# Kernel optimization log

Measured on AMD Instinct MI355X. Metric: run time of the kernel, lower is better.

## Reference

```python
import jax, jax.numpy as jnp
import numpy as np

T, B, D, H, NQ = 512, 256, 256, 256, 4  # note H == B is required by the original torch broadcasting


def setup_inputs() -> dict:
    key = jax.random.key(0)
    ks = jax.random.split(key, 9)
    inp = {"inputs": jax.random.normal(ks[0], (T, B, D), jnp.float32)}
    names = ["forget", "input", "update", "output"]
    for j, n in enumerate(names):
        inp[f"W_{n}"] = jax.random.normal(ks[1 + j], (NQ, D + H), jnp.float32) * 0.05
        inp[f"b_{n}"] = jnp.zeros((NQ,), jnp.float32)
        inp[f"phi_{n}"] = jax.random.uniform(ks[5 + j], (NQ,), jnp.float32, 0.0, 2.0 * np.pi)
    return inp


def _qgate(z, phi):
    # 4-qubit circuit on |0000>: RX(z_j) then trainable RX(phi_j) on each wire
    # (two RX on the same wire compose: angle theta_j = z_j + phi_j), then the
    # CNOT ring (0->1,1->2,2->3,3->0), then <Z_0>.
    # Heisenberg picture: conjugating Z_0 back through the CNOT ring gives
    # Z_0 -> Z_1 Z_2 Z_3, and on the product state <Z_j> = cos(theta_j), so
    # <Z_0> = cos(theta_1) * cos(theta_2) * cos(theta_3)  (wire 0 drops out).
    c = jnp.cos(z + phi)  # [B, 4]
    return c[:, 1] * c[:, 2] * c[:, 3]  # [B]


def reference(inputs, W_forget, b_forget, phi_forget, W_input, b_input, phi_input,
              W_update, b_update, phi_update, W_output, b_output, phi_output):
    bsz = inputs.shape[1]
    hx = jnp.zeros((bsz, H), inputs.dtype)
    cx = jnp.zeros((bsz, H), inputs.dtype)

    def step(carry, x):
        hx, cx = carry
        comb = jnp.concatenate([x, hx], axis=1)  # [B, D+H]
        f = jax.nn.sigmoid(_qgate(comb @ W_forget.T + b_forget, phi_forget))   # [B]
        i = jax.nn.sigmoid(_qgate(comb @ W_input.T + b_input, phi_input))      # [B]
        g = jnp.tanh(_qgate(comb @ W_update.T + b_update, phi_update))         # [B]
        o = jax.nn.sigmoid(_qgate(comb @ W_output.T + b_output, phi_output))   # [B]
        # [B] * [B,H] broadcasts the gate over the hidden axis (valid since H == B,
        # exactly matching the original torch semantics)
        cx = f * cx + i * g
        hx = o * jnp.tanh(cx)
        return (hx, cx), hx

    (hx, cx), outs = jax.lax.scan(step, (hx, cx), inputs)
    return outs, hx, cx
```

## Files before the change

### kernel.cpp

```cpp
#include <hip/hip_runtime.h>


#define T_DIM 512
#define B_DIM 256
#define D_DIM 256
#define H_DIM 256
#define DH    512
#define NG    16
#define XPAD  68

typedef float f32x4 __attribute__((ext_vector_type(4)));

__device__ __forceinline__ float fast_sigmoid(float x) {
    return 1.0f / (1.0f + __expf(-x));
}
__device__ __forceinline__ float fast_tanh(float x) {
    float e = __expf(2.0f * x);
    return (e - 1.0f) / (e + 1.0f);
}
template <int CTRL, int RM, int BM, bool BC>
__device__ __forceinline__ float dadd(float x) {
    return x + __int_as_float(
        __builtin_amdgcn_update_dpp(0, __float_as_int(x), CTRL, RM, BM, BC));
}
__device__ __forceinline__ float wsum(float x) {
    x = dadd<0x111, 0xf, 0xf, true >(x);
    x = dadd<0x112, 0xf, 0xf, true >(x);
    x = dadd<0x114, 0xf, 0xf, true >(x);
    x = dadd<0x118, 0xf, 0xf, true >(x);
    x = dadd<0x142, 0xa, 0xf, false>(x);
    x = dadd<0x143, 0xc, 0xf, false>(x);
    return x;
}
__device__ __forceinline__ float dpp_xor1(float x) {
    return __int_as_float(
        __builtin_amdgcn_update_dpp(0, __float_as_int(x), 0xB1, 0xf, 0xf, true));
}
__device__ __forceinline__ void lds_barrier() {
    __asm__ volatile("s_waitcnt lgkmcnt(0)\n\ts_barrier" ::: "memory");
}

__global__ __launch_bounds__(256) void zx_kernel(
    const float* __restrict__ x,
    const float* __restrict__ Wf, const float* __restrict__ Wi,
    const float* __restrict__ Wu, const float* __restrict__ Wo,
    const float* __restrict__ bf, const float* __restrict__ bi,
    const float* __restrict__ bu, const float* __restrict__ bo,
    const float* __restrict__ phf, const float* __restrict__ phi,
    const float* __restrict__ phu, const float* __restrict__ pho,
    float* __restrict__ zx)
{
    __shared__ float Xc[256][XPAD];
    __shared__ float Wc[NG][XPAD];
    const int tid = threadIdx.x;
    const int rt  = tid >> 2;
    const int qt  = tid & 3;

    const float* bv = (qt == 0) ? bf : (qt == 1) ? bi : (qt == 2) ? bu : bo;
    const float* pv = (qt == 0) ? phf : (qt == 1) ? phi : (qt == 2) ? phu : pho;
    float acc[4][4];
    #pragma unroll
    for (int j = 0; j < 4; ++j) {
        const float bj = bv[j] + pv[j];
        acc[0][j] = bj; acc[1][j] = bj; acc[2][j] = bj; acc[3][j] = bj;
    }

    const long base = (long)blockIdx.x * 256 * D_DIM;

    for (int c = 0; c < 4; ++c) {
        const int k0 = c * 64;
        #pragma unroll
        for (int it = 0; it < 16; ++it) {
            const int e = tid + it * 256;
            const int row = e >> 4, col4 = (e & 15) * 4;
            *(float4*)&Xc[row][col4] =
                *(const float4*)(x + base + (long)row * D_DIM + k0 + col4);
        }
        {
            const int q16 = tid >> 4, col4 = (tid & 15) * 4;
            const int g = q16 >> 2, qj = q16 & 3;
            const float* W = (g == 0) ? Wf : (g == 1) ? Wi : (g == 2) ? Wu : Wo;
            *(float4*)&Wc[q16][col4] = *(const float4*)(W + qj * DH + k0 + col4);
        }
        __syncthreads();

        #pragma unroll 4
        for (int kk = 0; kk < 16; ++kk) {
            const int k4 = kk * 4;
            float4 xv0 = *(float4*)&Xc[rt][k4];
            float4 xv1 = *(float4*)&Xc[rt +  64][k4];
            float4 xv2 = *(float4*)&Xc[rt + 128][k4];
            float4 xv3 = *(float4*)&Xc[rt + 192][k4];
            float4 wv0 = *(float4*)&Wc[4 * qt + 0][k4];
            float4 wv1 = *(float4*)&Wc[4 * qt + 1][k4];
            float4 wv2 = *(float4*)&Wc[4 * qt + 2][k4];
            float4 wv3 = *(float4*)&Wc[4 * qt + 3][k4];
            #pragma unroll
            for (int i = 0; i < 4; ++i) {
                const float4 xv = (i == 0) ? xv0 : (i == 1) ? xv1 : (i == 2) ? xv2 : xv3;
                acc[i][0] = fmaf(xv.x, wv0.x, fmaf(xv.y, wv0.y, fmaf(xv.z, wv0.z, fmaf(xv.w, wv0.w, acc[i][0]))));
                acc[i][1] = fmaf(xv.x, wv1.x, fmaf(xv.y, wv1.y, fmaf(xv.z, wv1.z, fmaf(xv.w, wv1.w, acc[i][1]))));
                acc[i][2] = fmaf(xv.x, wv2.x, fmaf(xv.y, wv2.y, fmaf(xv.z, wv2.z, fmaf(xv.w, wv2.w, acc[i][2]))));
                acc[i][3] = fmaf(xv.x, wv3.x, fmaf(xv.y, wv3.y, fmaf(xv.z, wv3.z, fmaf(xv.w, wv3.w, acc[i][3]))));
            }
        }
        __syncthreads();
    }

    const long orow = (long)blockIdx.x * 256;
    #pragma unroll
    for (int i = 0; i < 4; ++i) {
        *(float4*)&zx[(orow + rt + 64 * i) * NG + qt * 4] =
            make_float4(acc[i][0], acc[i][1], acc[i][2], acc[i][3]);
    }
}

__global__ __launch_bounds__(512) void rec_kernel(
    const float* __restrict__ Wf, const float* __restrict__ Wi,
    const float* __restrict__ Wu, const float* __restrict__ Wo,
    const float* __restrict__ zx,
    float* __restrict__ hv_tab,
    float* __restrict__ c_fin)
{
    __shared__ float Hbuf[2][H_DIM];
    __shared__ __align__(16) float zh_s[2][8];
    const int tid  = threadIdx.x;
    const int lane = tid & 63;
    const int wv   = tid >> 6;
    const int h    = tid >> 1;
    const int half = tid & 1;
    const int l4   = lane * 4;

    float4 WA = make_float4(0,0,0,0), WB = WA;
    if (wv < 6) {
        const int cA = 2 * wv, cB = cA + 1;
        const int gA = cA / 3, jA = cA % 3 + 1;
        const int gB = cB / 3, jB = cB % 3 + 1;
        const float* WgA = (gA == 0) ? Wf : (gA == 1) ? Wi : (gA == 2) ? Wu : Wo;
        const float* WgB = (gB == 0) ? Wf : (gB == 1) ? Wi : (gB == 2) ? Wu : Wo;
        WA = *(const float4*)(WgA + jA * DH + 256 + l4);
        WB = *(const float4*)(WgB + jB * DH + 256 + l4);
    }

    float C = 0.0f, Hprev = 0.0f;
    if (tid < H_DIM) Hbuf[1][tid] = 0.0f;
    __syncthreads();

    float4 za0, za1, zb0, zb1;
    {
        const float4* p0 = (const float4*)(zx + (long)h * NG) + half * 2;
        const float4* p1 = (const float4*)(zx + ((long)B_DIM + h) * NG) + half * 2;
        za0 = p0[0]; za1 = p0[1];
        zb0 = p1[0]; zb1 = p1[1];
    }

    auto step = [&](int t, float4& z0, float4& z1) {
        if (half) hv_tab[(long)(t - 1) * H_DIM + h] = Hprev;

        if (wv < 6) {
            const float4 Hv4 = *(const float4*)&Hbuf[(t + 1) & 1][l4];
            float pA = fmaf(WA.x, Hv4.x, fmaf(WA.y, Hv4.y, fmaf(WA.z, Hv4.z, WA.w * Hv4.w)));
            float pB = fmaf(WB.x, Hv4.x, fmaf(WB.y, Hv4.y, fmaf(WB.z, Hv4.z, WB.w * Hv4.w)));
            pA = wsum(pA);
            pB = wsum(pB);
            if (lane == 63) {
                const int cA = 2 * wv;
                zh_s[cA / 6][cA % 6]             = pA;
                zh_s[(cA + 1) / 6][(cA + 1) % 6] = pB;
            }
        }
        lds_barrier();

        const float4 ZA = *(const float4*)&zh_s[half][0];
        const float2 ZB = *(const float2*)&zh_s[half][4];
        const float c1 = __cosf(z0.y + ZA.x), c2 = __cosf(z0.z + ZA.y), c3 = __cosf(z0.w + ZA.z);
        const float c4 = __cosf(z1.y + ZA.w), c5 = __cosf(z1.z + ZB.x), c6 = __cosf(z1.w + ZB.y);
        const float pA = c1 * c2 * c3, pB = c4 * c5 * c6;
        float gA, gB;
        if (half == 0) { gA = fast_sigmoid(pA); gB = fast_sigmoid(pB); }
        else           { gA = fast_tanh(pA);    gB = fast_sigmoid(pB); }
        const float oA = dpp_xor1(gA);
        const float oB = dpp_xor1(gB);
        const float f_ = half ? oA : gA;
        const float i_ = half ? oB : gB;
        const float g_ = half ? gA : oA;
        const float o_ = half ? gB : oB;

        {
            const int tp = (t + 2 < T_DIM) ? (t + 2) : t;
            const float4* pp = (const float4*)(zx + ((long)tp * B_DIM + h) * NG) + half * 2;
            z0 = pp[0]; z1 = pp[1];
        }

        C = fmaf(f_, C, i_ * g_);
        const float Hnew = o_ * fast_tanh(C);
        if (half == 0) Hbuf[t & 1][h] = Hnew;
        Hprev = Hnew;
        lds_barrier();
    };

    for (int t = 0; t < T_DIM; t += 2) {
        step(t,     za0, za1);
        step(t + 1, zb0, zb1);
    }

    if (half) {
        hv_tab[(long)(T_DIM - 1) * H_DIM + h] = Hprev;
        c_fin[h] = C;
    }
}

__global__ __launch_bounds__(256) void bc_kernel(
    const float* __restrict__ hv_tab, const float* __restrict__ c_fin,
    float* __restrict__ out)
{
    const int blk  = blockIdx.x;
    const int w    = threadIdx.x >> 6;
    const int lane = threadIdx.x & 63;

    const float* src;
    long base;
    int rbase;
    if (blk < 4 * T_DIM) {
        const int t = blk >> 2;
        rbase = (blk & 3) * 64;
        src = hv_tab + (long)t * H_DIM;
        base = (long)t * (B_DIM * H_DIM);
    } else {
        const int k = blk - 4 * T_DIM;
        rbase = (k & 3) * 64;
        src = (k < 4) ? (hv_tab + (long)(T_DIM - 1) * H_DIM) : c_fin;
        base = (long)T_DIM * (B_DIM * H_DIM) + (k < 4 ? 0 : (long)B_DIM * H_DIM);
    }
    const f32x4 v = ((const f32x4*)src)[lane];
    #pragma unroll
    for (int it = 0; it < 16; ++it) {
        const int row = rbase + w + 4 * it;
        __builtin_nontemporal_store(
            v, (f32x4*)(out + base + (long)row * H_DIM) + lane);
    }
}

extern "C" void kernel_launch(void* const* d_in, const int* in_sizes, int n_in,
                              void* d_out, int out_size, void* d_ws, size_t ws_size,
                              hipStream_t stream) {
    (void)in_sizes; (void)n_in; (void)out_size; (void)ws_size;
    const float* x   = (const float*)d_in[0];
    const float* Wf  = (const float*)d_in[1];
    const float* bf  = (const float*)d_in[2];
    const float* phf = (const float*)d_in[3];
    const float* Wi  = (const float*)d_in[4];
    const float* bi  = (const float*)d_in[5];
    const float* phi = (const float*)d_in[6];
    const float* Wu  = (const float*)d_in[7];
    const float* bu  = (const float*)d_in[8];
    const float* phu = (const float*)d_in[9];
    const float* Wo  = (const float*)d_in[10];
    const float* bo  = (const float*)d_in[11];
    const float* pho = (const float*)d_in[12];

    float* zx     = (float*)d_ws;
    float* hv_pad = zx + (size_t)T_DIM * B_DIM * NG;
    float* hv_tab = hv_pad + H_DIM;
    float* c_fin  = hv_tab + (size_t)T_DIM * H_DIM;

    zx_kernel<<<T_DIM, 256, 0, stream>>>(
        x, Wf, Wi, Wu, Wo, bf, bi, bu, bo, phf, phi, phu, pho, zx);

    rec_kernel<<<1, 512, 0, stream>>>(
        Wf, Wi, Wu, Wo, zx, hv_tab, c_fin);

    bc_kernel<<<4 * T_DIM + 8, 256, 0, stream>>>(hv_tab, c_fin, (float*)d_out);
}
```

Measured before the change: 599.6 us.

## Fuse broadcast into recurrence kernel with chunked flag-based producer-consumer overlap

Merges the broadcast kernel into the recurrent kernel. Block 0 runs the serial recurrence and publishes a release flag after each 32-step chunk of hidden states. The other blocks spin on those flags and write the broadcast output while the recurrence is still running. The aim is to hide the large broadcast write traffic behind the latency-bound serial scan. In exchange it relies on all blocks being co-resident (risk of deadlock otherwise), and the stores from consumer blocks may contend with the recurrence block.

```diff
diff --git a/kernel.cpp b/kernel.cpp
--- a/kernel.cpp
+++ b/kernel.cpp
@@ -8,6 +8,8 @@
 #define DH    512
 #define NG    16
 #define XPAD  68
+#define CHUNK 32
+#define NCHUNK (T_DIM / CHUNK)
 
 typedef float f32x4 __attribute__((ext_vector_type(4)));
 
@@ -39,6 +41,16 @@
 __device__ __forceinline__ void lds_barrier() {
     __asm__ volatile("s_waitcnt lgkmcnt(0)\n\ts_barrier" ::: "memory");
 }
+__device__ __forceinline__ void wait_flag(const int* f) {
+    if (threadIdx.x == 0) {
+        while (__hip_atomic_load(f, __ATOMIC_ACQUIRE,
+                                 __HIP_MEMORY_SCOPE_AGENT) == 0) {
+            __builtin_amdgcn_s_sleep(32);
+        }
+    }
+    __syncthreads();
+    __threadfence();
+}
 
 __global__ __launch_bounds__(256) void zx_kernel(
     const float* __restrict__ x,
@@ -48,13 +60,15 @@
     const float* __restrict__ bu, const float* __restrict__ bo,
     const float* __restrict__ phf, const float* __restrict__ phi,
     const float* __restrict__ phu, const float* __restrict__ pho,
-    float* __restrict__ zx)
+    float* __restrict__ zx, int* __restrict__ flags)
 {
     __shared__ float Xc[256][XPAD];
     __shared__ float Wc[NG][XPAD];
     const int tid = threadIdx.x;
     const int rt  = tid >> 2;
     const int qt  = tid & 3;
+
+    if (blockIdx.x == 0 && tid < NCHUNK) flags[tid] = 0;
 
     const float* bv = (qt == 0) ? bf : (qt == 1) ? bi : (qt == 2) ? bu : bo;
     const float* pv = (qt == 0) ? phf : (qt == 1) ? phi : (qt == 2) ? phu : pho;
@@ -115,16 +129,54 @@
     }
 }
 
-__global__ __launch_bounds__(512) void rec_kernel(
+__global__ __launch_bounds__(512, 8) void rec_bc_kernel(
     const float* __restrict__ Wf, const float* __restrict__ Wi,
     const float* __restrict__ Wu, const float* __restrict__ Wo,
     const float* __restrict__ zx,
     float* __restrict__ hv_tab,
-    float* __restrict__ c_fin)
+    float* __restrict__ c_fin,
+    int* __restrict__ flags,
+    float* __restrict__ out)
 {
+    const int tid  = threadIdx.x;
+
+    if (blockIdx.x != 0) {
+        const int lane = tid & 63;
+        const int w    = tid >> 6;
+
+        if (blockIdx.x <= 256) {
+            const int tb0 = 2 * ((int)blockIdx.x - 1);
+            wait_flag(&flags[tb0 >> 5]);
+            #pragma unroll
+            for (int tt = 0; tt < 2; ++tt) {
+                const int tb = tb0 + tt;
+                const f32x4 v = ((const f32x4*)(hv_tab + (long)tb * H_DIM))[lane];
+                const long base = (long)tb * (B_DIM * H_DIM);
+                #pragma unroll
+                for (int it = 0; it < 32; ++it) {
+                    const int row = w + 8 * it;
+                    __builtin_nontemporal_store(
+                        v, (f32x4*)(out + base + (long)row * H_DIM) + lane);
+                }
+            }
+        } else {
+            wait_flag(&flags[NCHUNK - 1]);
+            const f32x4 vh = ((const f32x4*)(hv_tab + (long)(T_DIM - 1) * H_DIM))[lane];
+            const f32x4 vc = ((const f32x4*)c_fin)[lane];
+            const long bh = (long)T_DIM * (B_DIM * H_DIM);
+            const long bc = bh + (long)B_DIM * H_DIM;
+            #pragma unroll
+            for (int it = 0; it < 32; ++it) {
+                const int row = w + 8 * it;
+                __builtin_nontemporal_store(vh, (f32x4*)(out + bh + (long)row * H_DIM) + lane);
+                __builtin_nontemporal_store(vc, (f32x4*)(out + bc + (long)row * H_DIM) + lane);
+            }
+        }
+        return;
+    }
+
     __shared__ float Hbuf[2][H_DIM];
     __shared__ __align__(16) float zh_s[2][8];
-    const int tid  = threadIdx.x;
     const int lane = tid & 63;
     const int wv   = tid >> 6;
     const int h    = tid >> 1;
@@ -202,42 +254,27 @@
     for (int t = 0; t < T_DIM; t += 2) {
         step(t,     za0, za1);
         step(t + 1, zb0, zb1);
+        if (t > 0 && (t & 31) == 0) {
+            __asm__ volatile("s_waitcnt vmcnt(0)" ::: "memory");
+            __syncthreads();
+            if (tid == 0) {
+                __threadfence();
+                __hip_atomic_store(&flags[(t >> 5) - 1], 1,
+                                   __ATOMIC_RELEASE, __HIP_MEMORY_SCOPE_AGENT);
+            }
+        }
     }
 
     if (half) {
         hv_tab[(long)(T_DIM - 1) * H_DIM + h] = Hprev;
         c_fin[h] = C;
     }
-}
-
-__global__ __launch_bounds__(256) void bc_kernel(
-    const float* __restrict__ hv_tab, const float* __restrict__ c_fin,
-    float* __restrict__ out)
-{
-    const int blk  = blockIdx.x;
-    const int w    = threadIdx.x >> 6;
-    const int lane = threadIdx.x & 63;
-
-    const float* src;
-    long base;
-    int rbase;
-    if (blk < 4 * T_DIM) {
-        const int t = blk >> 2;
-        rbase = (blk & 3) * 64;
-        src = hv_tab + (long)t * H_DIM;
-        base = (long)t * (B_DIM * H_DIM);
-    } else {
-        const int k = blk - 4 * T_DIM;
-        rbase = (k & 3) * 64;
-        src = (k < 4) ? (hv_tab + (long)(T_DIM - 1) * H_DIM) : c_fin;
-        base = (long)T_DIM * (B_DIM * H_DIM) + (k < 4 ? 0 : (long)B_DIM * H_DIM);
-    }
-    const f32x4 v = ((const f32x4*)src)[lane];
-    #pragma unroll
-    for (int it = 0; it < 16; ++it) {
-        const int row = rbase + w + 4 * it;
-        __builtin_nontemporal_store(
-            v, (f32x4*)(out + base + (long)row * H_DIM) + lane);
+    __asm__ volatile("s_waitcnt vmcnt(0)" ::: "memory");
+    __syncthreads();
+    if (tid == 0) {
+        __threadfence();
+        __hip_atomic_store(&flags[NCHUNK - 1], 1,
+                           __ATOMIC_RELEASE, __HIP_MEMORY_SCOPE_AGENT);
     }
 }
 
@@ -263,12 +300,11 @@
     float* hv_pad = zx + (size_t)T_DIM * B_DIM * NG;
     float* hv_tab = hv_pad + H_DIM;
     float* c_fin  = hv_tab + (size_t)T_DIM * H_DIM;
+    int*   flags  = (int*)(c_fin + H_DIM);
 
     zx_kernel<<<T_DIM, 256, 0, stream>>>(
-        x, Wf, Wi, Wu, Wo, bf, bi, bu, bo, phf, phi, phu, pho, zx);
-
-    rec_kernel<<<1, 512, 0, stream>>>(
-        Wf, Wi, Wu, Wo, zx, hv_tab, c_fin);
-
-    bc_kernel<<<4 * T_DIM + 8, 256, 0, stream>>>(hv_tab, c_fin, (float*)d_out);
-}
+        x, Wf, Wi, Wu, Wo, bf, bi, bu, bo, phf, phi, phu, pho, zx, flags);
+
+    rec_bc_kernel<<<1 + B_DIM + 1, 512, 0, stream>>>(
+        Wf, Wi, Wu, Wo, zx, hv_tab, c_fin, flags, (float*)d_out);
+}
```

New measurement: 891.0 us. +48.6%, slower.
